# Optimization experiments

Hardware: AMD Instinct MI355X
Metric: run time of the kernel (lower is better)

Reference implementation:

```python
import jax, jax.numpy as jnp
import numpy as np


def setup_inputs() -> dict:
    key = jax.random.key(0)
    k1, k2 = jax.random.split(key)
    x = jax.random.normal(k1, (8, 512, 32, 14, 14), dtype=jnp.float32)
    # Conv1d(in=1, out=1, kernel=5, bias=False) weight, torch layout (O, I, K)
    conv_w = jax.random.normal(k2, (1, 1, 5), dtype=jnp.float32) * 0.2
    return {"x": x, "conv_w": conv_w}


def reference(x, conv_w):
    # x: (N, C, T, H, W)
    N, C, T = x.shape[:3]
    PAD = 2  # k=5, padding=k//2
    # Global average pool over H, W -> (N, C, T)
    gap = x.mean(axis=(3, 4))
    # Original loops over T applying Conv1d over the channel axis per timestep.
    # Batched equivalent: fold T into the batch dim -> (N*T, 1, C)
    seq = gap.transpose(0, 2, 1).reshape(N * T, 1, C)
    y = jax.lax.conv_general_dilated(
        seq, conv_w, window_strides=(1,), padding=[(PAD, PAD)],
        dimension_numbers=("NCH", "OIH", "NCH"))  # (N*T, 1, C)
    att = jax.nn.sigmoid(y.reshape(N, T, C).transpose(0, 2, 1))  # (N, C, T)
    return att[..., None, None]  # (N, C, T, 1, 1)
```

## Files before the change

### kernel.cpp

```cpp
#include <hip/hip_runtime.h>
#include <hip/hip_bf16.h>


#define HW 196
#define HW4 49

__global__ void gap_kernel(const float* __restrict__ x,
                           float* __restrict__ gap,
                           int total_rows) {
    const int waves_per_block = blockDim.x >> 6;
    const int row  = blockIdx.x * waves_per_block + (threadIdx.x >> 6);
    const int lane = threadIdx.x & 63;
    if (row >= total_rows) return;

    const float4* p = reinterpret_cast<const float4*>(x + (size_t)row * HW);
    float s = 0.0f;
    if (lane < HW4) {
        float4 v = p[lane];
        s = (v.x + v.y) + (v.z + v.w);
    }
    #pragma unroll
    for (int off = 32; off > 0; off >>= 1)
        s += __shfl_down(s, off, 64);

    if (lane == 0) gap[row] = s * (1.0f / 196.0f);
}

__global__ void conv_sig_kernel(const float* __restrict__ gap,
                                const float* __restrict__ w,
                                float* __restrict__ out,
                                int N, int C, int T) {
    const int idx = blockIdx.x * blockDim.x + threadIdx.x;
    const int total = N * C * T;
    if (idx >= total) return;

    const int t = idx % T;
    const int c = (idx / T) % C;
    const int n = idx / (T * C);

    const float w0 = w[0], w1 = w[1], w2 = w[2], w3 = w[3], w4 = w[4];

    const float* g = gap + ((size_t)n * C) * T + t;
    float acc = 0.0f;
    if (c >= 2)      acc += w0 * g[(c - 2) * T];
    if (c >= 1)      acc += w1 * g[(c - 1) * T];
                     acc += w2 * g[c * T];
    if (c + 1 < C)   acc += w3 * g[(c + 1) * T];
    if (c + 2 < C)   acc += w4 * g[(c + 2) * T];

    out[idx] = 1.0f / (1.0f + __expf(-acc));
}

extern "C" void kernel_launch(void* const* d_in, const int* in_sizes, int n_in,
                              void* d_out, int out_size, void* d_ws, size_t ws_size,
                              hipStream_t stream) {
    const float* x = (const float*)d_in[0];
    const float* w = (const float*)d_in[1];
    float* out = (float*)d_out;
    float* gap = (float*)d_ws;

    const int N = 8, C = 512, T = 32;
    const int total_rows = N * C * T;

    const int waves_per_block = 4;
    const int blocks1 = (total_rows + waves_per_block - 1) / waves_per_block;
    gap_kernel<<<blocks1, waves_per_block * 64, 0, stream>>>(x, gap, total_rows);

    const int threads2 = 256;
    const int blocks2 = (total_rows + threads2 - 1) / threads2;
    conv_sig_kernel<<<blocks2, threads2, 0, stream>>>(gap, w, out, N, C, T);
}
```

Baseline: 26.95 us.

## Fuse pooling and channel conv-sigmoid into one kernel per (n,t) block

Merges the global-average-pool kernel and the conv1d+sigmoid kernel into one kernel. Each block handles one (n,t) pair, reduces all 512 channel rows into shared memory, then applies the 5-tap channel convolution and sigmoid. This removes the second launch and the global round trip for the pooled values. In exchange the grid shrinks to 256 large blocks, which may reduce memory-level parallelism on the streaming read.

```diff
diff --git a/kernel.cpp b/kernel.cpp
--- a/kernel.cpp
+++ b/kernel.cpp
@@ -4,51 +4,49 @@
 
 #define HW 196
 #define HW4 49
+#define C_ 512
+#define T_ 32
 
-__global__ void gap_kernel(const float* __restrict__ x,
-                           float* __restrict__ gap,
-                           int total_rows) {
-    const int waves_per_block = blockDim.x >> 6;
-    const int row  = blockIdx.x * waves_per_block + (threadIdx.x >> 6);
+__global__ __launch_bounds__(1024) void fused_attn_kernel(
+        const float* __restrict__ x,
+        const float* __restrict__ w,
+        float* __restrict__ out) {
+    const int b    = blockIdx.x;
+    const int t    = b & (T_ - 1);
+    const int n    = b >> 5;
+    const int wave = threadIdx.x >> 6;
     const int lane = threadIdx.x & 63;
-    if (row >= total_rows) return;
 
-    const float4* p = reinterpret_cast<const float4*>(x + (size_t)row * HW);
-    float s = 0.0f;
-    if (lane < HW4) {
-        float4 v = p[lane];
-        s = (v.x + v.y) + (v.z + v.w);
+    __shared__ float gap[C_];
+
+    const float* xb = x + ((size_t)(n * C_) * T_ + t) * HW;
+
+    #pragma unroll 4
+    for (int i = 0; i < 32; ++i) {
+        const int c = (wave << 5) + i;
+        const float4* p = reinterpret_cast<const float4*>(xb + (size_t)c * (T_ * HW));
+        float s = 0.0f;
+        if (lane < HW4) {
+            float4 v = p[lane];
+            s = (v.x + v.y) + (v.z + v.w);
+        }
+        #pragma unroll
+        for (int off = 32; off > 0; off >>= 1)
+            s += __shfl_down(s, off, 64);
+        if (lane == 0) gap[c] = s * (1.0f / 196.0f);
     }
-    #pragma unroll
-    for (int off = 32; off > 0; off >>= 1)
-        s += __shfl_down(s, off, 64);
+    __syncthreads();
 
-    if (lane == 0) gap[row] = s * (1.0f / 196.0f);
-}
-
-__global__ void conv_sig_kernel(const float* __restrict__ gap,
-                                const float* __restrict__ w,
-                                float* __restrict__ out,
-                                int N, int C, int T) {
-    const int idx = blockIdx.x * blockDim.x + threadIdx.x;
-    const int total = N * C * T;
-    if (idx >= total) return;
-
-    const int t = idx % T;
-    const int c = (idx / T) % C;
-    const int n = idx / (T * C);
-
-    const float w0 = w[0], w1 = w[1], w2 = w[2], w3 = w[3], w4 = w[4];
-
-    const float* g = gap + ((size_t)n * C) * T + t;
-    float acc = 0.0f;
-    if (c >= 2)      acc += w0 * g[(c - 2) * T];
-    if (c >= 1)      acc += w1 * g[(c - 1) * T];
-                     acc += w2 * g[c * T];
-    if (c + 1 < C)   acc += w3 * g[(c + 1) * T];
-    if (c + 2 < C)   acc += w4 * g[(c + 2) * T];
-
-    out[idx] = 1.0f / (1.0f + __expf(-acc));
+    const int c = threadIdx.x;
+    if (c < C_) {
+        const float w0 = w[0], w1 = w[1], w2 = w[2], w3 = w[3], w4 = w[4];
+        float acc = w2 * gap[c];
+        if (c >= 2)     acc += w0 * gap[c - 2];
+        if (c >= 1)     acc += w1 * gap[c - 1];
+        if (c + 1 < C_) acc += w3 * gap[c + 1];
+        if (c + 2 < C_) acc += w4 * gap[c + 2];
+        out[((size_t)n * C_ + c) * T_ + t] = 1.0f / (1.0f + __expf(-acc));
+    }
 }
 
 extern "C" void kernel_launch(void* const* d_in, const int* in_sizes, int n_in,
@@ -57,16 +55,7 @@
     const float* x = (const float*)d_in[0];
     const float* w = (const float*)d_in[1];
     float* out = (float*)d_out;
-    float* gap = (float*)d_ws;
 
-    const int N = 8, C = 512, T = 32;
-    const int total_rows = N * C * T;
-
-    const int waves_per_block = 4;
-    const int blocks1 = (total_rows + waves_per_block - 1) / waves_per_block;
-    gap_kernel<<<blocks1, waves_per_block * 64, 0, stream>>>(x, gap, total_rows);
-
-    const int threads2 = 256;
-    const int blocks2 = (total_rows + threads2 - 1) / threads2;
-    conv_sig_kernel<<<blocks2, threads2, 0, stream>>>(gap, w, out, N, C, T);
+    const int N = 8;
+    fused_attn_kernel<<<N * T_, 1024, 0, stream>>>(x, w, out);
 }
```

Result: faster. 26.10 us (-3.2%).

## Stream GAP input contiguously per block and reduce rows through shared memory

Applied to the files above, without the earlier changes.

The pooling kernel now gives each 256-thread block 64 contiguous rows. Threads stream float4s fully coalesced across row boundaries instead of leaving 15 of 64 lanes idle per row. Partial sums go to LDS, and 64 threads then each serially sum 49 values for one row. This aims to raise memory-bandwidth utilisation and cut block count, but it adds a barrier, 12.5KB of LDS per block, and a serial reduction tail done by one wave.

```diff
diff --git a/kernel.cpp b/kernel.cpp
--- a/kernel.cpp
+++ b/kernel.cpp
@@ -2,28 +2,34 @@
 #include <hip/hip_bf16.h>
 
 
-#define HW 196
-#define HW4 49
+#define ROWS_PER_BLOCK 64
+#define F4_PER_ROW 49
+#define F4_PER_BLOCK (ROWS_PER_BLOCK * F4_PER_ROW)
+#define THREADS_A 256
 
-__global__ void gap_kernel(const float* __restrict__ x,
-                           float* __restrict__ gap,
-                           int total_rows) {
-    const int waves_per_block = blockDim.x >> 6;
-    const int row  = blockIdx.x * waves_per_block + (threadIdx.x >> 6);
-    const int lane = threadIdx.x & 63;
-    if (row >= total_rows) return;
+__global__ __launch_bounds__(THREADS_A) void gap_kernel(
+        const float* __restrict__ x,
+        float* __restrict__ gap) {
+    __shared__ float part[F4_PER_BLOCK];
 
-    const float4* p = reinterpret_cast<const float4*>(x + (size_t)row * HW);
-    float s = 0.0f;
-    if (lane < HW4) {
-        float4 v = p[lane];
-        s = (v.x + v.y) + (v.z + v.w);
+    const int tid = threadIdx.x;
+    const float4* p = reinterpret_cast<const float4*>(x) +
+                      (size_t)blockIdx.x * F4_PER_BLOCK;
+
+    #pragma unroll
+    for (int j = tid; j < F4_PER_BLOCK; j += THREADS_A) {
+        float4 v = p[j];
+        part[j] = (v.x + v.y) + (v.z + v.w);
     }
-    #pragma unroll
-    for (int off = 32; off > 0; off >>= 1)
-        s += __shfl_down(s, off, 64);
+    __syncthreads();
 
-    if (lane == 0) gap[row] = s * (1.0f / 196.0f);
+    if (tid < ROWS_PER_BLOCK) {
+        const float* q = &part[tid * F4_PER_ROW];
+        float s = 0.0f;
+        #pragma unroll
+        for (int k = 0; k < F4_PER_ROW; ++k) s += q[k];
+        gap[(size_t)blockIdx.x * ROWS_PER_BLOCK + tid] = s * (1.0f / 196.0f);
+    }
 }
 
 __global__ void conv_sig_kernel(const float* __restrict__ gap,
@@ -41,10 +47,9 @@
     const float w0 = w[0], w1 = w[1], w2 = w[2], w3 = w[3], w4 = w[4];
 
     const float* g = gap + ((size_t)n * C) * T + t;
-    float acc = 0.0f;
+    float acc = w2 * g[c * T];
     if (c >= 2)      acc += w0 * g[(c - 2) * T];
     if (c >= 1)      acc += w1 * g[(c - 1) * T];
-                     acc += w2 * g[c * T];
     if (c + 1 < C)   acc += w3 * g[(c + 1) * T];
     if (c + 2 < C)   acc += w4 * g[(c + 2) * T];
 
@@ -61,12 +66,11 @@
 
     const int N = 8, C = 512, T = 32;
     const int total_rows = N * C * T;
+    const int blocksA = total_rows / ROWS_PER_BLOCK;
 
-    const int waves_per_block = 4;
-    const int blocks1 = (total_rows + waves_per_block - 1) / waves_per_block;
-    gap_kernel<<<blocks1, waves_per_block * 64, 0, stream>>>(x, gap, total_rows);
+    gap_kernel<<<blocksA, THREADS_A, 0, stream>>>(x, gap);
 
-    const int threads2 = 256;
-    const int blocks2 = (total_rows + threads2 - 1) / threads2;
-    conv_sig_kernel<<<blocks2, threads2, 0, stream>>>(gap, w, out, N, C, T);
+    const int threadsB = 256;
+    const int blocksB = (total_rows + threadsB - 1) / threadsB;
+    conv_sig_kernel<<<blocksB, threadsB, 0, stream>>>(gap, w, out, N, C, T);
 }
```

Measured after the change: 24.25 us. 1.11x faster.
